# Performance work log

Hardware: AMD Instinct MI355X
Metric: run time of the kernel (lower is better)

Reference implementation:

```python
import jax, jax.numpy as jnp
import numpy as np

B, C = 2097152, 15   # batch, num_category (15 hardcoded in original via sum_term/15)
EPS = 1e-32
ALPHA = 0.1


def setup_inputs() -> dict:
    key = jax.random.key(0)
    k1, k2 = jax.random.split(key)
    output = jax.random.normal(k1, (B, C), dtype=jnp.float32)
    labels = jax.random.randint(k2, (B, C), 0, 2).astype(jnp.float32)  # 0/1 targets
    return {"output": output, "labels": labels}


def reference(output, labels):
    # outs_sig = sigmoid(output[:, :C])
    sig = jax.nn.sigmoid(output)                      # [B, C]

    # Per-category AUC-hinge penalty. The original builds the full
    # num_pos x num_neg outer-difference matrix and takes its mean, which
    # equals 1 - mean(pos) + mean(neg); empty sides contribute 0 (matching
    # the num_pos==0 / num_neg==0 branches where trans_* = 0).
    pos = labels                                      # 1 where label==1
    neg = 1.0 - labels                                # 1 where label==0
    npos = jnp.sum(pos, axis=0)                       # [C]
    nneg = jnp.sum(neg, axis=0)                       # [C]
    mean_pos = jnp.where(npos > 0, jnp.sum(sig * pos, axis=0) / jnp.maximum(npos, 1.0), 0.0)
    mean_neg = jnp.where(nneg > 0, jnp.sum(sig * neg, axis=0) / jnp.maximum(nneg, 1.0), 0.0)
    penalty = 1.0 - mean_pos + mean_neg               # [C]
    sum_term = jnp.sum(penalty)

    # CEL: applies sigmoid AGAIN to outs_sig (faithful to original double sigmoid)
    s2 = jax.nn.sigmoid(sig)
    cel = (-jnp.mean(labels * jnp.log(s2 + EPS))
           - jnp.mean((1.0 - labels) * jnp.log(1.0 - s2 + EPS)))

    cls = cel + ALPHA * (sum_term / 15.0)
    return (cls, ALPHA * penalty[-1])
```

## Files before the change

kernel.cpp:

```cpp
#include <hip/hip_runtime.h>


#define CATS 15
#define NBLOCKS 960
#define NTHREADS 256
#define NSUMS (3 * CATS + 1)
#define PF 10
#define ITERS 32

typedef float vf4 __attribute__((ext_vector_type(4)));

__device__ __forceinline__ vf4 ntload4(const vf4* p) {
    return __builtin_nontemporal_load(p);
}

__device__ __forceinline__ float softplus_neg_unit(float s) {
    const float c0 = 0.69314718f, c1 = -0.5f, c2 = 0.125f, c4 = -0.0048853f;
    float s2 = s * s;
    return c0 + fmaf(c1, s, fmaf(c2, s2, c4 * s2 * s2));
}

__device__ __forceinline__ void accum_elem(float x, float l,
                                           float& ssig, float& spos, float& snp,
                                           float& scel) {
    float e   = __expf(-x);
    float sig = __builtin_amdgcn_rcpf(1.0f + e);
    ssig += sig;
    spos = fmaf(sig, l, spos);
    snp  += l;
    scel += softplus_neg_unit(sig);
}

__global__ __launch_bounds__(NTHREADS) void mauch_main(
    const float* __restrict__ outp, const float* __restrict__ labp,
    float* __restrict__ ws, int nFloat4)
{
    const int t = blockIdx.x * blockDim.x + threadIdx.x;
    const int stride = gridDim.x * blockDim.x;

    float ssig[4] = {0.f, 0.f, 0.f, 0.f};
    float spos[4] = {0.f, 0.f, 0.f, 0.f};
    float snp[4]  = {0.f, 0.f, 0.f, 0.f};
    float scel = 0.f;

    const vf4* o4 = (const vf4*)outp;
    const vf4* l4 = (const vf4*)labp;

    if (nFloat4 == ITERS * stride) {
        vf4 ob[PF], lb[PF];
#pragma unroll
        for (int p = 0; p < PF; ++p) {
            ob[p] = ntload4(o4 + t + p * stride);
            lb[p] = ntload4(l4 + t + p * stride);
        }
#pragma unroll
        for (int i = 0; i < ITERS; ++i) {
            vf4 ov = ob[i % PF];
            vf4 lv = lb[i % PF];
            if (i + PF < ITERS) {
                ob[i % PF] = ntload4(o4 + t + (i + PF) * stride);
                lb[i % PF] = ntload4(l4 + t + (i + PF) * stride);
            }
#pragma unroll
            for (int j = 0; j < 4; ++j)
                accum_elem(ov[j], lv[j], ssig[j], spos[j], snp[j], scel);
        }
    } else {
        for (int f = t; f < nFloat4; f += stride) {
            vf4 ov = ntload4(o4 + f);
            vf4 lv = ntload4(l4 + f);
#pragma unroll
            for (int j = 0; j < 4; ++j)
                accum_elem(ov[j], lv[j], ssig[j], spos[j], snp[j], scel);
        }
    }

    __shared__ float red[NSUMS];
    for (int i = threadIdx.x; i < NSUMS; i += blockDim.x) red[i] = 0.f;
    __syncthreads();

    int base = (4 * t) % CATS;
#pragma unroll
    for (int j = 0; j < 4; ++j) {
        int c = base + j; if (c >= CATS) c -= CATS;
        atomicAdd(&red[c],            ssig[j]);
        atomicAdd(&red[CATS + c],     spos[j]);
        atomicAdd(&red[2 * CATS + c], snp[j]);
    }
    atomicAdd(&red[3 * CATS], scel);
    __syncthreads();

    if (threadIdx.x < NSUMS) atomicAdd(&ws[threadIdx.x], red[threadIdx.x]);
}

__global__ void mauch_final(const float* __restrict__ ws, float* __restrict__ out,
                            float invBC, float rowsB)
{
    if (threadIdx.x == 0 && blockIdx.x == 0) {
        float sum_term = 0.f, pen_last = 0.f;
        float tot_ssig = 0.f, tot_spos = 0.f;
#pragma unroll
        for (int c = 0; c < CATS; ++c) {
            float ssig = ws[c];
            float sp   = ws[CATS + c];
            float np   = ws[2 * CATS + c];
            float nn   = rowsB - np;
            float sneg = ssig - sp;
            tot_ssig += ssig;
            tot_spos += sp;
            float mp = (np > 0.f) ? sp   / fmaxf(np, 1.f) : 0.f;
            float mn = (nn > 0.f) ? sneg / fmaxf(nn, 1.f) : 0.f;
            float pen = 1.f - mp + mn;
            sum_term += pen;
            if (c == CATS - 1) pen_last = pen;
        }
        float cel = (ws[3 * CATS] + (tot_ssig - tot_spos)) * invBC;
        out[0] = cel + 0.1f * (sum_term / 15.f);
        out[1] = 0.1f * pen_last;
    }
}

extern "C" void kernel_launch(void* const* d_in, const int* in_sizes, int n_in,
                              void* d_out, int out_size, void* d_ws, size_t ws_size,
                              hipStream_t stream) {
    const float* outp = (const float*)d_in[0];
    const float* labp = (const float*)d_in[1];
    float* out = (float*)d_out;
    float* ws  = (float*)d_ws;

    const int total   = in_sizes[0];
    const int nFloat4 = total / 4;
    const float rowsB = (float)(total / CATS);
    const float invBC = 1.0f / (float)total;

    hipMemsetAsync(ws, 0, NSUMS * sizeof(float), stream);

    mauch_main<<<NBLOCKS, NTHREADS, 0, stream>>>(outp, labp, ws, nFloat4);
    mauch_final<<<1, 64, 0, stream>>>(ws, out, invBC, rowsB);
}
```

Measured before the change: 251.0 us.

## Stage loads via global_load_lds DMA and write per-block partials instead of atomics

Replaces register-prefetched nontemporal loads with direct global-to-LDS DMA loads, double-buffered per wave, and doubles the grid while halving iterations per thread. When the workspace is large enough, each block writes its partial sums to its own slot instead of using global atomics, and the final kernel reduces them with 1024 threads, which also removes the memset. This is meant to cut register pressure, raise occupancy and avoid atomic contention and the extra memset launch. In exchange it depends on hand-written waitcnt assembly being correct and gives up the deep ten-deep register prefetch for a two-stage LDS pipeline.

```diff
diff --git a/kernel.cpp b/kernel.cpp
--- a/kernel.cpp
+++ b/kernel.cpp
@@ -2,16 +2,24 @@
 
 
 #define CATS 15
-#define NBLOCKS 960
+#define NBLOCKS 1920
 #define NTHREADS 256
 #define NSUMS (3 * CATS + 1)
-#define PF 10
-#define ITERS 32
+#define ITERS 16
+#define DEPTH 2
+#define PLD 2048
 
 typedef float vf4 __attribute__((ext_vector_type(4)));
 
 __device__ __forceinline__ vf4 ntload4(const vf4* p) {
     return __builtin_nontemporal_load(p);
+}
+
+__device__ __forceinline__ void dma16(const vf4* g, vf4* lds) {
+    __builtin_amdgcn_global_load_lds(
+        (const __attribute__((address_space(1))) void*)g,
+        (__attribute__((address_space(3))) void*)lds,
+        16, 0, 0);
 }
 
 __device__ __forceinline__ float softplus_neg_unit(float s) {
@@ -31,12 +39,14 @@
     scel += softplus_neg_unit(sig);
 }
 
-__global__ __launch_bounds__(NTHREADS) void mauch_main(
+__global__ __launch_bounds__(NTHREADS, 8) void mauch_main(
     const float* __restrict__ outp, const float* __restrict__ labp,
-    float* __restrict__ ws, int nFloat4)
+    float* __restrict__ ws, int nFloat4, int mode)
 {
     const int t = blockIdx.x * blockDim.x + threadIdx.x;
     const int stride = gridDim.x * blockDim.x;
+    const int lane = threadIdx.x & 63;
+    const int wv   = threadIdx.x >> 6;
 
     float ssig[4] = {0.f, 0.f, 0.f, 0.f};
     float spos[4] = {0.f, 0.f, 0.f, 0.f};
@@ -46,20 +56,25 @@
     const vf4* o4 = (const vf4*)outp;
     const vf4* l4 = (const vf4*)labp;
 
+    __shared__ vf4 stage[NTHREADS / 64][DEPTH][2][64];
+
     if (nFloat4 == ITERS * stride) {
-        vf4 ob[PF], lb[PF];
 #pragma unroll
-        for (int p = 0; p < PF; ++p) {
-            ob[p] = ntload4(o4 + t + p * stride);
-            lb[p] = ntload4(l4 + t + p * stride);
+        for (int p = 0; p < DEPTH; ++p) {
+            dma16(o4 + t + p * stride, &stage[wv][p][0][0]);
+            dma16(l4 + t + p * stride, &stage[wv][p][1][0]);
         }
 #pragma unroll
         for (int i = 0; i < ITERS; ++i) {
-            vf4 ov = ob[i % PF];
-            vf4 lv = lb[i % PF];
-            if (i + PF < ITERS) {
-                ob[i % PF] = ntload4(o4 + t + (i + PF) * stride);
-                lb[i % PF] = ntload4(l4 + t + (i + PF) * stride);
+            const int s = i % DEPTH;
+            if (i <= ITERS - DEPTH) asm volatile("s_waitcnt vmcnt(2)" ::: "memory");
+            else                    asm volatile("s_waitcnt vmcnt(0)" ::: "memory");
+            vf4 ov = stage[wv][s][0][lane];
+            vf4 lv = stage[wv][s][1][lane];
+            asm volatile("s_waitcnt lgkmcnt(0)" ::: "memory");
+            if (i + DEPTH < ITERS) {
+                dma16(o4 + t + (i + DEPTH) * stride, &stage[wv][s][0][0]);
+                dma16(l4 + t + (i + DEPTH) * stride, &stage[wv][s][1][0]);
             }
 #pragma unroll
             for (int j = 0; j < 4; ++j)
@@ -90,23 +105,44 @@
     atomicAdd(&red[3 * CATS], scel);
     __syncthreads();
 
-    if (threadIdx.x < NSUMS) atomicAdd(&ws[threadIdx.x], red[threadIdx.x]);
+    if (threadIdx.x < NSUMS) {
+        if (mode) ws[threadIdx.x * PLD + blockIdx.x] = red[threadIdx.x];
+        else      atomicAdd(&ws[threadIdx.x], red[threadIdx.x]);
+    }
 }
 
-__global__ void mauch_final(const float* __restrict__ ws, float* __restrict__ out,
-                            float invBC, float rowsB)
+__global__ __launch_bounds__(1024) void mauch_final(
+    const float* __restrict__ ws, float* __restrict__ out,
+    float invBC, float rowsB, int mode)
 {
-    if (threadIdx.x == 0 && blockIdx.x == 0) {
+    __shared__ float sums[NSUMS];
+    const int lane = threadIdx.x & 63;
+    const int wv   = threadIdx.x >> 6;
+
+    if (mode) {
+        for (int k = wv; k < NSUMS; k += 16) {
+            float v = 0.f;
+            for (int b = lane; b < NBLOCKS; b += 64) v += ws[k * PLD + b];
+#pragma unroll
+            for (int off = 32; off; off >>= 1) v += __shfl_down(v, off, 64);
+            if (lane == 0) sums[k] = v;
+        }
+    } else {
+        if (threadIdx.x < NSUMS) sums[threadIdx.x] = ws[threadIdx.x];
+    }
+    __syncthreads();
+
+    if (threadIdx.x == 0) {
         float sum_term = 0.f, pen_last = 0.f;
         float tot_ssig = 0.f, tot_spos = 0.f;
 #pragma unroll
         for (int c = 0; c < CATS; ++c) {
-            float ssig = ws[c];
-            float sp   = ws[CATS + c];
-            float np   = ws[2 * CATS + c];
-            float nn   = rowsB - np;
-            float sneg = ssig - sp;
-            tot_ssig += ssig;
+            float ssigc = sums[c];
+            float sp    = sums[CATS + c];
+            float np    = sums[2 * CATS + c];
+            float nn    = rowsB - np;
+            float sneg  = ssigc - sp;
+            tot_ssig += ssigc;
             tot_spos += sp;
             float mp = (np > 0.f) ? sp   / fmaxf(np, 1.f) : 0.f;
             float mn = (nn > 0.f) ? sneg / fmaxf(nn, 1.f) : 0.f;
@@ -114,7 +150,7 @@
             sum_term += pen;
             if (c == CATS - 1) pen_last = pen;
         }
-        float cel = (ws[3 * CATS] + (tot_ssig - tot_spos)) * invBC;
+        float cel = (sums[3 * CATS] + (tot_ssig - tot_spos)) * invBC;
         out[0] = cel + 0.1f * (sum_term / 15.f);
         out[1] = 0.1f * pen_last;
     }
@@ -133,8 +169,10 @@
     const float rowsB = (float)(total / CATS);
     const float invBC = 1.0f / (float)total;
 
-    hipMemsetAsync(ws, 0, NSUMS * sizeof(float), stream);
+    const size_t needed = (size_t)NSUMS * PLD * sizeof(float);
+    const int mode = (ws_size >= needed) ? 1 : 0;
+    if (!mode) hipMemsetAsync(ws, 0, NSUMS * sizeof(float), stream);
 
-    mauch_main<<<NBLOCKS, NTHREADS, 0, stream>>>(outp, labp, ws, nFloat4);
-    mauch_final<<<1, 64, 0, stream>>>(ws, out, invBC, rowsB);
+    mauch_main<<<NBLOCKS, NTHREADS, 0, stream>>>(outp, labp, ws, nFloat4, mode);
+    mauch_final<<<1, 1024, 0, stream>>>(ws, out, invBC, rowsB, mode);
 }
```

Result: slower. 349.2 us (+39.1%).
